# Kernel optimization log

Measured on AMD Instinct MI355X. Metric: run time of the kernel, lower is better.

The kernel has to match this reference:

```python
import jax, jax.numpy as jnp
import numpy as np


def setup_inputs() -> dict:
    key = jax.random.key(0)
    k1, k2 = jax.random.split(key)
    B, N, D = 8, 256, 128
    x = jax.random.normal(k1, (B, N, D), dtype=jnp.float32)
    # Dense edge layer: maps 2D -> D (concat of the two node embeddings).
    W = jax.random.normal(k2, (2 * D, D), dtype=jnp.float32) * (1.0 / np.sqrt(2 * D))
    b = jnp.zeros((D,), dtype=jnp.float32)
    return {"x": x, "W": W, "b": b}


def reference(x, W, b):
    # PairwiseEdgeEmbeddings: e[b,i,j] = concat(x[b,i], x[b,j])  -> (B,N,N,2D)
    # Edge layer: relu(e @ W + b)                                 -> (B,N,N,D)
    # Faithful but efficient: concat @ W == x_i @ W1 + x_j @ W2 with W=[W1;W2],
    # avoiding materializing the (B,N,N,2D) concat tensor.
    D = x.shape[-1]
    W1, W2 = W[:D], W[D:]
    a = jnp.einsum('bnd,df->bnf', x, W1)  # contribution of node i
    c = jnp.einsum('bnd,df->bnf', x, W2)  # contribution of node j
    edges = jax.nn.relu(a[:, :, None, :] + c[:, None, :, :] + b)  # (B,N,N,D)
    # Reduce layer: sum over j -> node embeddings (B,N,D)
    return edges.sum(axis=2)
```

## Files before the change

### kernel.cpp

```cpp
#include <hip/hip_runtime.h>

typedef float f32x4 __attribute__((ext_vector_type(4)));

#define B_ 8
#define N_ 256
#define D_ 128

__global__ __launch_bounds__(256) void gemm_ac_kernel(
    const float* __restrict__ x, const float* __restrict__ W,
    const float* __restrict__ bias, float* __restrict__ A, float* __restrict__ C) {
    __shared__ float  xs[8][D_];
    __shared__ float4 Ws[32][64];

    const int tid  = threadIdx.x;
    const int r0   = blockIdx.x * 8;
    const int rq   = tid >> 6;
    const int cq   = tid & 63;
    const int halfC = cq >> 5;
    const int f    = (cq * 4) & 127;

    {
        const int row = tid >> 5;
        const int dq  = tid & 31;
        reinterpret_cast<float4*>(&xs[row][0])[dq] =
            *reinterpret_cast<const float4*>(x + (size_t)(r0 + row) * D_ + dq * 4);
    }

    float4 acc0 = make_float4(0.f, 0.f, 0.f, 0.f);
    float4 acc1 = make_float4(0.f, 0.f, 0.f, 0.f);

    for (int chunk = 0; chunk < 4; ++chunk) {
        if (chunk) __syncthreads();
        #pragma unroll
        for (int k = 0; k < 8; ++k) {
            const int id = k * 256 + tid;
            const int dd = id >> 6;
            const int cg = id & 63;
            const int srow = chunk * 32 + dd + ((cg >> 5) << 7);
            Ws[dd][cg] = *reinterpret_cast<const float4*>(
                W + (size_t)srow * D_ + (cg & 31) * 4);
        }
        __syncthreads();

        const int dbase = chunk * 32;
        #pragma unroll
        for (int dd = 0; dd < 32; ++dd) {
            const float4 wv = Ws[dd][cq];
            const float x0 = xs[rq * 2    ][dbase + dd];
            const float x1 = xs[rq * 2 + 1][dbase + dd];
            acc0.x += x0 * wv.x; acc0.y += x0 * wv.y;
            acc0.z += x0 * wv.z; acc0.w += x0 * wv.w;
            acc1.x += x1 * wv.x; acc1.y += x1 * wv.y;
            acc1.z += x1 * wv.z; acc1.w += x1 * wv.w;
        }
    }

    const int row0 = r0 + rq * 2;
    if (halfC) {
        *reinterpret_cast<float4*>(C + (size_t)row0 * D_ + f)       = acc0;
        *reinterpret_cast<float4*>(C + (size_t)(row0 + 1) * D_ + f) = acc1;
    } else {
        const float4 bv = *reinterpret_cast<const float4*>(bias + f);
        acc0.x += bv.x; acc0.y += bv.y; acc0.z += bv.z; acc0.w += bv.w;
        acc1.x += bv.x; acc1.y += bv.y; acc1.z += bv.z; acc1.w += bv.w;
        *reinterpret_cast<float4*>(A + (size_t)row0 * D_ + f)       = acc0;
        *reinterpret_cast<float4*>(A + (size_t)(row0 + 1) * D_ + f) = acc1;
    }
}

__global__ __launch_bounds__(256) void reduce_edges_kernel(
    const float* __restrict__ A, const float* __restrict__ C,
    float* __restrict__ out) {
    __shared__ f32x4 part[8][4][32];

    const int blk = blockIdx.x;
    const int b   = blk >> 6;
    const int i0  = (blk & 63) * 4;
    const int tid = threadIdx.x;
    const int fq  = tid & 31;
    const int jg  = tid >> 5;

    f32x4 av[4], acc[4];
    const f32x4 zero = {0.f, 0.f, 0.f, 0.f};
    #pragma unroll
    for (int r = 0; r < 4; ++r) {
        av[r] = *reinterpret_cast<const f32x4*>(
            A + ((size_t)(b * N_ + i0 + r)) * D_ + fq * 4);
        acc[r] = zero;
    }

    const f32x4* __restrict__ Cv =
        reinterpret_cast<const f32x4*>(C + (size_t)b * N_ * D_) +
        (size_t)(jg * 32) * 32 + fq;
    #pragma unroll 4
    for (int j = 0; j < 32; ++j) {
        const f32x4 cv = Cv[(size_t)j * 32];
        #pragma unroll
        for (int r = 0; r < 4; ++r) {
            f32x4 t = av[r] + cv;
            t = __builtin_elementwise_max(t, zero);
            acc[r] += t;
        }
    }

    #pragma unroll
    for (int r = 0; r < 4; ++r) part[jg][r][fq] = acc[r];
    __syncthreads();

    if (tid < 128) {
        const int rr = tid >> 5, ff = tid & 31;
        f32x4 s = part[0][rr][ff];
        #pragma unroll
        for (int k = 1; k < 8; ++k) s += part[k][rr][ff];
        *reinterpret_cast<f32x4*>(
            out + ((size_t)(b * N_ + i0 + rr)) * D_ + ff * 4) = s;
    }
}

__global__ __launch_bounds__(128) void fused_naive_kernel(
    const float* __restrict__ x, const float* __restrict__ W,
    const float* __restrict__ bias, float* __restrict__ out) {
    const int r = blockIdx.x;
    const int b = r / N_;
    const int f = threadIdx.x;
    const float* __restrict__ xi = x + (size_t)r * D_;
    float a = bias[f];
    for (int d = 0; d < D_; ++d) a += xi[d] * W[d * D_ + f];
    float acc = 0.0f;
    const float* __restrict__ xb = x + (size_t)b * N_ * D_;
    for (int j = 0; j < N_; ++j) {
        const float* __restrict__ xj = xb + (size_t)j * D_;
        float c = 0.0f;
        for (int d = 0; d < D_; ++d) c += xj[d] * W[(D_ + d) * D_ + f];
        acc += fmaxf(a + c, 0.0f);
    }
    out[(size_t)r * D_ + f] = acc;
}

extern "C" void kernel_launch(void* const* d_in, const int* in_sizes, int n_in,
                              void* d_out, int out_size, void* d_ws, size_t ws_size,
                              hipStream_t stream) {
    const float* x    = (const float*)d_in[0];
    const float* W    = (const float*)d_in[1];
    const float* bias = (const float*)d_in[2];
    float* out = (float*)d_out;

    const size_t elems = (size_t)B_ * N_ * D_;
    const size_t need  = 2 * elems * sizeof(float);

    if (ws_size >= need) {
        float* A = (float*)d_ws;
        float* C = A + elems;
        gemm_ac_kernel<<<(B_ * N_) / 8, 256, 0, stream>>>(x, W, bias, A, C);
        reduce_edges_kernel<<<(B_ * N_) / 4, 256, 0, stream>>>(A, C, out);
    } else {
        fused_naive_kernel<<<B_ * N_, D_, 0, stream>>>(x, W, bias, out);
    }
}
```

Before: 19.28 us.

## Fuse GEMM and edge reduction into one cooperative kernel with grid sync

Replaces the two-kernel sequence (projection GEMM, then pairwise relu-sum reduction) with a single cooperative launch of 256 blocks of 512 threads that computes A and C, keeps A in shared memory, grid-syncs, then performs the reduction. This removes a kernel launch boundary and the global round-trip for A. The cost is a grid-wide barrier, half the threads idle during the GEMM phase, and reliance on cooperative launch, with the old two-kernel path kept as a fallback if that launch fails.

```diff
diff --git a/kernel.cpp b/kernel.cpp
--- a/kernel.cpp
+++ b/kernel.cpp
@@ -1,10 +1,128 @@
 #include <hip/hip_runtime.h>
+#include <hip/hip_cooperative_groups.h>
+
+namespace cg = cooperative_groups;
 
 typedef float f32x4 __attribute__((ext_vector_type(4)));
 
 #define B_ 8
 #define N_ 256
 #define D_ 128
+
+__global__ __launch_bounds__(512, 1) void fused_coop_kernel(
+    const float* __restrict__ x, const float* __restrict__ W,
+    const float* __restrict__ bias, float* __restrict__ C,
+    float* __restrict__ out) {
+
+    __shared__ float  xs[8][D_];
+    __shared__ float4 Ws[32][64];
+    __shared__ f32x4  As[8][32];
+    __shared__ f32x4  part[8][8][32];
+
+    const int tid  = threadIdx.x;
+    const int bid  = blockIdx.x;
+    const int b    = bid & 7;
+    const int slot = bid >> 3;
+    const int r0   = b * N_ + slot * 8;
+
+    if (tid < 256) {
+        const int row = tid >> 5, dq = tid & 31;
+        reinterpret_cast<float4*>(&xs[row][0])[dq] =
+            *reinterpret_cast<const float4*>(x + (size_t)(r0 + row) * D_ + dq * 4);
+    }
+
+    const int rq    = (tid >> 6) & 3;
+    const int cq    = tid & 63;
+    const int halfC = cq >> 5;
+    const int f     = (cq * 4) & 127;
+
+    float4 acc0 = make_float4(0.f, 0.f, 0.f, 0.f);
+    float4 acc1 = make_float4(0.f, 0.f, 0.f, 0.f);
+
+    for (int chunk = 0; chunk < 4; ++chunk) {
+        __syncthreads();
+        #pragma unroll
+        for (int k = 0; k < 4; ++k) {
+            const int id = k * 512 + tid;
+            const int dd = id >> 6;
+            const int cg = id & 63;
+            const int srow = chunk * 32 + dd + ((cg >> 5) << 7);
+            Ws[dd][cg] = *reinterpret_cast<const float4*>(
+                W + (size_t)srow * D_ + (cg & 31) * 4);
+        }
+        __syncthreads();
+
+        if (tid < 256) {
+            const int dbase = chunk * 32;
+            #pragma unroll
+            for (int dd = 0; dd < 32; ++dd) {
+                const float4 wv = Ws[dd][cq];
+                const float x0 = xs[rq * 2    ][dbase + dd];
+                const float x1 = xs[rq * 2 + 1][dbase + dd];
+                acc0.x += x0 * wv.x; acc0.y += x0 * wv.y;
+                acc0.z += x0 * wv.z; acc0.w += x0 * wv.w;
+                acc1.x += x1 * wv.x; acc1.y += x1 * wv.y;
+                acc1.z += x1 * wv.z; acc1.w += x1 * wv.w;
+            }
+        }
+    }
+
+    if (tid < 256) {
+        const int row0 = r0 + rq * 2;
+        if (halfC) {
+            *reinterpret_cast<float4*>(C + (size_t)row0 * D_ + f)       = acc0;
+            *reinterpret_cast<float4*>(C + (size_t)(row0 + 1) * D_ + f) = acc1;
+        } else {
+            const float4 bv = *reinterpret_cast<const float4*>(bias + f);
+            acc0.x += bv.x; acc0.y += bv.y; acc0.z += bv.z; acc0.w += bv.w;
+            acc1.x += bv.x; acc1.y += bv.y; acc1.z += bv.z; acc1.w += bv.w;
+            As[rq * 2    ][f >> 2] = f32x4{acc0.x, acc0.y, acc0.z, acc0.w};
+            As[rq * 2 + 1][f >> 2] = f32x4{acc1.x, acc1.y, acc1.z, acc1.w};
+        }
+    }
+
+    cg::this_grid().sync();
+
+    {
+        const int fq = tid & 31;
+        const int rg = (tid >> 5) & 1;
+        const int jg = tid >> 6;
+        const f32x4 zero = {0.f, 0.f, 0.f, 0.f};
+
+        f32x4 av[4], acc[4];
+        #pragma unroll
+        for (int r = 0; r < 4; ++r) {
+            av[r]  = As[rg * 4 + r][fq];
+            acc[r] = zero;
+        }
+
+        const f32x4* __restrict__ Cb =
+            reinterpret_cast<const f32x4*>(C) +
+            ((size_t)b * N_ + jg * 32) * 32 + fq;
+        #pragma unroll 4
+        for (int jj = 0; jj < 32; ++jj) {
+            const f32x4 cv = Cb[(size_t)jj * 32];
+            #pragma unroll
+            for (int r = 0; r < 4; ++r) {
+                f32x4 t = av[r] + cv;
+                t = __builtin_elementwise_max(t, zero);
+                acc[r] += t;
+            }
+        }
+
+        #pragma unroll
+        for (int r = 0; r < 4; ++r) part[jg][rg * 4 + r][fq] = acc[r];
+    }
+    __syncthreads();
+
+    if (tid < 256) {
+        const int row = tid >> 5, ff = tid & 31;
+        f32x4 s = part[0][row][ff];
+        #pragma unroll
+        for (int k = 1; k < 8; ++k) s += part[k][row][ff];
+        reinterpret_cast<f32x4*>(out)[(size_t)(r0 + row) * 32 + ff] = s;
+    }
+}
 
 __global__ __launch_bounds__(256) void gemm_ac_kernel(
     const float* __restrict__ x, const float* __restrict__ W,
@@ -146,13 +264,18 @@
     float* out = (float*)d_out;
 
     const size_t elems = (size_t)B_ * N_ * D_;
-    const size_t need  = 2 * elems * sizeof(float);
-
-    if (ws_size >= need) {
-        float* A = (float*)d_ws;
-        float* C = A + elems;
-        gemm_ac_kernel<<<(B_ * N_) / 8, 256, 0, stream>>>(x, W, bias, A, C);
-        reduce_edges_kernel<<<(B_ * N_) / 4, 256, 0, stream>>>(A, C, out);
+
+    if (ws_size >= 2 * elems * sizeof(float)) {
+        float* C = (float*)d_ws;
+        float* A = C + elems;
+
+        void* args[] = {(void*)&x, (void*)&W, (void*)&bias, (void*)&C, (void*)&out};
+        hipError_t err = hipLaunchCooperativeKernel(
+            (const void*)fused_coop_kernel, dim3(256), dim3(512), args, 0, stream);
+        if (err != hipSuccess) {
+            gemm_ac_kernel<<<(B_ * N_) / 8, 256, 0, stream>>>(x, W, bias, A, C);
+            reduce_edges_kernel<<<(B_ * N_) / 4, 256, 0, stream>>>(A, C, out);
+        }
     } else {
         fused_naive_kernel<<<B_ * N_, D_, 0, stream>>>(x, W, bias, out);
     }
```

Result: slower. 50.72 us (+163.1%).
